# Optimization experiments

Hardware: AMD Instinct MI355X
Metric: run time of the kernel (lower is better)

The kernel has to match this reference:

```python
import jax, jax.numpy as jnp
import numpy as np
import math

N_EMBD = 1024
N_HEAD = 16
B, T = 4, 2048

def setup_inputs() -> dict:
    key = jax.random.key(0)
    k1, k2, k3, k4 = jax.random.split(key, 4)
    x = jax.random.normal(k1, (B, T, N_EMBD), dtype=jnp.float32)
    # torch Linear weights: [out, in]; init scale ~1/sqrt(in)
    s = 1.0 / math.sqrt(N_EMBD)
    W_attn = jax.random.normal(k2, (3 * N_EMBD, N_EMBD), dtype=jnp.float32) * s
    W_proj = jax.random.normal(k3, (N_EMBD, N_EMBD), dtype=jnp.float32) * s
    b_proj = jax.random.normal(k4, (N_EMBD,), dtype=jnp.float32) * s
    return {"x": x, "W_attn": W_attn, "W_proj": W_proj, "b_proj": b_proj}

def reference(x, W_attn, W_proj, b_proj):
    Bx, Tx, C = x.shape
    hd = C // N_HEAD
    qkv = jnp.einsum('btc,oc->bto', x, W_attn)  # [B,T,3C]
    q, k, v = jnp.split(qkv, 3, axis=2)
    # [B, H, T, hd]
    q = q.reshape(Bx, Tx, N_HEAD, hd).transpose(0, 2, 1, 3)
    k = k.reshape(Bx, Tx, N_HEAD, hd).transpose(0, 2, 1, 3)
    v = v.reshape(Bx, Tx, N_HEAD, hd).transpose(0, 2, 1, 3)
    # NOTE: source divides by (1/sqrt(hd)) => MULTIPLIES by sqrt(hd). Faithful.
    att = jnp.einsum('bhqd,bhkd->bhqk', q, k) * jnp.sqrt(jnp.float32(hd))
    causal = jnp.tril(jnp.ones((Tx, Tx), dtype=bool))
    att = jnp.where(causal[None, None, :, :], att, -jnp.inf)
    att = jax.nn.softmax(att, axis=-1)
    y = jnp.einsum('bhqk,bhkd->bhqd', att, v)
    y = y.transpose(0, 2, 1, 3).reshape(Bx, Tx, C)
    y = jnp.einsum('btc,oc->bto', y, W_proj) + b_proj
    return y  # dropout is identity in eval
```

## Files before the change

### kernel.cpp

```cpp
#include <hip/hip_runtime.h>
#include <math.h>

#define BATCH 4
#define TSEQ  2048
#define CEMB  1024
#define NHEAD 16
#define HD    64
#define MROWS (BATCH * TSEQ)
#define QSCALE 11.5415603271f

typedef _Float16 half8 __attribute__((ext_vector_type(8)));
typedef _Float16 half4 __attribute__((ext_vector_type(4)));
typedef _Float16 half2 __attribute__((ext_vector_type(2)));
typedef float    floatx4 __attribute__((ext_vector_type(4)));

#define GLOBAL_AS __attribute__((address_space(1)))
#define LDS_AS    __attribute__((address_space(3)))

__device__ __forceinline__ void lds_dma16(const _Float16* g, _Float16* l) {
    __builtin_amdgcn_global_load_lds((const GLOBAL_AS unsigned int*)g,
                                     (LDS_AS unsigned int*)l, 16, 0, 0);
}

__device__ __forceinline__ float fast_exp2(float x) {
    float r; asm("v_exp_f32 %0, %1" : "=v"(r) : "v"(x)); return r;
}

__device__ __forceinline__ half4 pack4(float a0, float a1, float a2, float a3) {
    half2 lo = __builtin_bit_cast(half2, __builtin_amdgcn_cvt_pkrtz(a0, a1));
    half2 hi = __builtin_bit_cast(half2, __builtin_amdgcn_cvt_pkrtz(a2, a3));
    return (half4){lo[0], lo[1], hi[0], hi[1]};
}

__global__ __launch_bounds__(256)
void cvt_fp16(const float* __restrict__ x, const float* __restrict__ wa,
              const float* __restrict__ wp, _Float16* __restrict__ x16,
              _Float16* __restrict__ wa16, _Float16* __restrict__ wp16)
{
    const int n1 = (BATCH * TSEQ * CEMB) / 4;
    const int n2 = (3 * CEMB * CEMB) / 4;
    int i = blockIdx.x * 256 + threadIdx.x;
    const float* src; _Float16* dst; int j;
    if (i < n1)            { src = x;  dst = x16;  j = i; }
    else if (i < n1 + n2)  { src = wa; dst = wa16; j = i - n1; }
    else                   { src = wp; dst = wp16; j = i - n1 - n2; }
    float4 v = ((const float4*)src)[j];
    half4 h = { (_Float16)v.x, (_Float16)v.y, (_Float16)v.z, (_Float16)v.w };
    ((half4*)dst)[j] = h;
}

__device__ __forceinline__ void stage32(const _Float16* __restrict__ gbase,
                                        _Float16* __restrict__ lds,
                                        int row0, int kk, int tid)
{
#pragma unroll
    for (int p = 0; p < 2; ++p) {
        int ci  = p * 256 + tid;
        int row = ci >> 2, pcc = ci & 3;
        int c   = pcc ^ (row & 3);
        lds_dma16(gbase + (size_t)(row0 + row) * CEMB + kk + c * 8, lds + ci * 8);
    }
}

__global__ __launch_bounds__(256)
void qkv_gemm(const _Float16* __restrict__ A, const _Float16* __restrict__ B,
              _Float16* __restrict__ q16, _Float16* __restrict__ k16,
              _Float16* __restrict__ v16)
{
    __shared__ __align__(16) _Float16 smem[16384];
    const int tid = threadIdx.x, lane = tid & 63, wave = tid >> 6;
    const int wm = wave & 1, wn = wave >> 1;
    const int L  = blockIdx.x + 24 * blockIdx.y;
    const int jj = L >> 3;
    const int m0 = ((L & 7) + 8 * (jj & 7)) * 128;
    const int n0 = (jj >> 3) * 128;
    const int l15 = lane & 15, quad = lane >> 4;

    floatx4 acc[4][4];
#pragma unroll
    for (int i = 0; i < 4; ++i)
#pragma unroll
        for (int j = 0; j < 4; ++j) acc[i][j] = (floatx4){0.f, 0.f, 0.f, 0.f};

    stage32(A, smem, m0, 0, tid);
    stage32(B, smem + 8192, n0, 0, tid);
    for (int kt = 0; kt < 32; ++kt) {
        const int cur = kt & 1;
        _Float16* Asc = smem + cur * 4096;
        _Float16* Bsc = smem + 8192 + cur * 4096;
        __syncthreads();
        if (kt < 31) {
            stage32(A, smem + (cur ^ 1) * 4096, m0, (kt + 1) * 32, tid);
            stage32(B, smem + 8192 + (cur ^ 1) * 4096, n0, (kt + 1) * 32, tid);
        }
        half8 af[4], bf[4];
#pragma unroll
        for (int mt = 0; mt < 4; ++mt) {
            int row = wm * 64 + mt * 16 + l15;
            af[mt] = *(const half8*)(Asc + row * 32 + (quad ^ (row & 3)) * 8);
        }
#pragma unroll
        for (int nt = 0; nt < 4; ++nt) {
            int row = wn * 64 + nt * 16 + l15;
            bf[nt] = *(const half8*)(Bsc + row * 32 + (quad ^ (row & 3)) * 8);
        }
#pragma unroll
        for (int mt = 0; mt < 4; ++mt)
#pragma unroll
            for (int nt = 0; nt < 4; ++nt)
                acc[mt][nt] = __builtin_amdgcn_mfma_f32_16x16x32_f16(af[mt], bf[nt], acc[mt][nt], 0, 0, 0);
    }

    __syncthreads();
    const int rbase = quad << 2;
    if (n0 < 2 * CEMB) {
        const float scale = (n0 < CEMB) ? QSCALE : 1.0f;
#pragma unroll
        for (int mt = 0; mt < 4; ++mt)
#pragma unroll
            for (int nt = 0; nt < 4; ++nt)
#pragma unroll
                for (int r = 0; r < 4; ++r) {
                    int t = wm * 64 + mt * 16 + rbase + r;
                    int n = wn * 64 + nt * 16 + l15;
                    int pc = (n >> 3) ^ (t & 15);
                    smem[t * 128 + pc * 8 + (n & 7)] = (_Float16)(acc[mt][nt][r] * scale);
                }
        __syncthreads();
        const int chunk = tid & 7;
#pragma unroll
        for (int i = 0; i < 8; ++i) {
            int gr = (tid >> 3) + i * 32;
            int seg = gr >> 7, t = gr & 127;
            int pc = (seg * 8 + chunk) ^ (t & 15);
            half8 v = *(const half8*)(smem + t * 128 + pc * 8);
            int gm = m0 + t, b = gm >> 11, tt = gm & (TSEQ - 1);
            int gnb = n0 + seg * 64;
            _Float16* dst;
            if (n0 < CEMB) {
                int h = gnb >> 6;
                dst = q16 + (((size_t)(b * NHEAD + h)) * TSEQ + tt) * HD;
            } else {
                int h = (gnb - CEMB) >> 6;
                dst = k16 + (((size_t)(b * NHEAD + h)) * TSEQ + tt) * HD;
            }
            *(half8*)(dst + chunk * 8) = v;
        }
    } else {
#pragma unroll
        for (int mt = 0; mt < 4; ++mt)
#pragma unroll
            for (int nt = 0; nt < 4; ++nt)
#pragma unroll
                for (int r = 0; r < 4; ++r) {
                    int t = wm * 64 + mt * 16 + rbase + r;
                    int n = wn * 64 + nt * 16 + l15;
                    int pc = (t >> 3) ^ (n & 15);
                    smem[n * 128 + pc * 8 + (t & 7)] = (_Float16)acc[mt][nt][r];
                }
        __syncthreads();
        const int chunk = tid & 15;
        const int b = m0 >> 11, tblk = m0 & (TSEQ - 1);
#pragma unroll
        for (int i = 0; i < 8; ++i) {
            int row = (tid >> 4) + i * 16;
            int pc = chunk ^ (row & 15);
            half8 v = *(const half8*)(smem + row * 128 + pc * 8);
            int c2 = n0 - 2 * CEMB + row;
            int h = c2 >> 6, d = c2 & 63;
            *(half8*)(v16 + (((size_t)(b * NHEAD + h)) * HD + d) * TSEQ + tblk + chunk * 8) = v;
        }
    }
}

__device__ __forceinline__ void attn_tile(
    const half8& qf0, const half8& qf1,
    float& m_i, float& l_i, floatx4 (&o)[4],
    const _Float16* __restrict__ Ks, const _Float16* __restrict__ Vs,
    bool domask, int l15, int quad, int relq)
{
    floatx4 s[4];
#pragma unroll
    for (int nt = 0; nt < 4; ++nt) {
        int row = nt * 16 + l15;
        int pc0 = quad ^ (row & 7);
        half8 kf0 = *(const half8*)(Ks + row * 64 + pc0 * 8);
        half8 kf1 = *(const half8*)(Ks + row * 64 + (pc0 ^ 4) * 8);
        floatx4 z = (floatx4){0.f, 0.f, 0.f, 0.f};
        z = __builtin_amdgcn_mfma_f32_16x16x32_f16(kf0, qf0, z, 0, 0, 0);
        z = __builtin_amdgcn_mfma_f32_16x16x32_f16(kf1, qf1, z, 0, 0, 0);
        s[nt] = z;
    }
    if (domask) {
#pragma unroll
        for (int nt = 0; nt < 4; ++nt)
#pragma unroll
            for (int r = 0; r < 4; ++r)
                if (nt * 16 + quad * 4 + r > relq) s[nt][r] = -INFINITY;
    }
    float pmax = -INFINITY;
#pragma unroll
    for (int nt = 0; nt < 4; ++nt)
        pmax = fmaxf(pmax, fmaxf(fmaxf(s[nt][0], s[nt][1]), fmaxf(s[nt][2], s[nt][3])));
    if (!__all(pmax <= m_i)) {
        float mx = fmaxf(m_i, pmax);
        mx = fmaxf(mx, __shfl_xor(mx, 16, 64));
        mx = fmaxf(mx, __shfl_xor(mx, 32, 64));
        float alpha = fast_exp2(m_i - mx);
        m_i = mx;
        l_i *= alpha;
#pragma unroll
        for (int mt = 0; mt < 4; ++mt)
#pragma unroll
            for (int r = 0; r < 4; ++r) o[mt][r] *= alpha;
    }
    float rs = 0.f;
    half4 p[4];
#pragma unroll
    for (int nt = 0; nt < 4; ++nt) {
        float p0 = fast_exp2(s[nt][0] - m_i), p1 = fast_exp2(s[nt][1] - m_i);
        float p2 = fast_exp2(s[nt][2] - m_i), p3 = fast_exp2(s[nt][3] - m_i);
        rs += (p0 + p1) + (p2 + p3);
        p[nt] = pack4(p0, p1, p2, p3);
    }
    l_i += rs;
#pragma unroll
    for (int mt = 0; mt < 4; ++mt) {
        int d = mt * 16 + l15;
#pragma unroll
        for (int nt = 0; nt < 4; ++nt) {
            int pc = (2 * nt + (quad >> 1)) ^ (d & 7);
            half4 vf = *(const half4*)(Vs + d * 64 + pc * 8 + (quad & 1) * 4);
            o[mt] = __builtin_amdgcn_mfma_f32_16x16x16f16(vf, p[nt], o[mt], 0, 0, 0);
        }
    }
}

__device__ __forceinline__ void attn_tile2(
    const half8& qA0, const half8& qA1, const half8& qB0, const half8& qB1,
    float& mAi, float& lAi, floatx4 (&oA)[4],
    float& mBi, float& lBi, floatx4 (&oB)[4],
    const _Float16* __restrict__ Ks, const _Float16* __restrict__ Vs,
    bool maskA, int l15, int quad, int relq)
{
    floatx4 sA[4], sB[4];
#pragma unroll
    for (int nt = 0; nt < 4; ++nt) {
        int row = nt * 16 + l15;
        int pc0 = quad ^ (row & 7);
        half8 kf0 = *(const half8*)(Ks + row * 64 + pc0 * 8);
        half8 kf1 = *(const half8*)(Ks + row * 64 + (pc0 ^ 4) * 8);
        floatx4 zA = (floatx4){0.f, 0.f, 0.f, 0.f};
        floatx4 zB = (floatx4){0.f, 0.f, 0.f, 0.f};
        zA = __builtin_amdgcn_mfma_f32_16x16x32_f16(kf0, qA0, zA, 0, 0, 0);
        zB = __builtin_amdgcn_mfma_f32_16x16x32_f16(kf0, qB0, zB, 0, 0, 0);
        zA = __builtin_amdgcn_mfma_f32_16x16x32_f16(kf1, qA1, zA, 0, 0, 0);
        zB = __builtin_amdgcn_mfma_f32_16x16x32_f16(kf1, qB1, zB, 0, 0, 0);
        sA[nt] = zA; sB[nt] = zB;
    }
    if (maskA) {
#pragma unroll
        for (int nt = 0; nt < 4; ++nt)
#pragma unroll
            for (int r = 0; r < 4; ++r)
                if (nt * 16 + quad * 4 + r > relq) sA[nt][r] = -INFINITY;
    }
    float pA = -INFINITY, pB = -INFINITY;
#pragma unroll
    for (int nt = 0; nt < 4; ++nt) {
        pA = fmaxf(pA, fmaxf(fmaxf(sA[nt][0], sA[nt][1]), fmaxf(sA[nt][2], sA[nt][3])));
        pB = fmaxf(pB, fmaxf(fmaxf(sB[nt][0], sB[nt][1]), fmaxf(sB[nt][2], sB[nt][3])));
    }
    if (!__all((pA <= mAi) && (pB <= mBi))) {
        float mxA = fmaxf(mAi, pA), mxB = fmaxf(mBi, pB);
        mxA = fmaxf(mxA, __shfl_xor(mxA, 16, 64));
        mxB = fmaxf(mxB, __shfl_xor(mxB, 16, 64));
        mxA = fmaxf(mxA, __shfl_xor(mxA, 32, 64));
        mxB = fmaxf(mxB, __shfl_xor(mxB, 32, 64));
        float alA = fast_exp2(mAi - mxA);
        float alB = fast_exp2(mBi - mxB);
        mAi = mxA; mBi = mxB;
        lAi *= alA; lBi *= alB;
#pragma unroll
        for (int mt = 0; mt < 4; ++mt)
#pragma unroll
            for (int r = 0; r < 4; ++r) { oA[mt][r] *= alA; oB[mt][r] *= alB; }
    }
    float rsA = 0.f, rsB = 0.f;
    half4 pAh[4], pBh[4];
#pragma unroll
    for (int nt = 0; nt < 4; ++nt) {
        float a0 = fast_exp2(sA[nt][0] - mAi), b0 = fast_exp2(sB[nt][0] - mBi);
        float a1 = fast_exp2(sA[nt][1] - mAi), b1 = fast_exp2(sB[nt][1] - mBi);
        float a2 = fast_exp2(sA[nt][2] - mAi), b2 = fast_exp2(sB[nt][2] - mBi);
        float a3 = fast_exp2(sA[nt][3] - mAi), b3 = fast_exp2(sB[nt][3] - mBi);
        rsA += (a0 + a1) + (a2 + a3);
        rsB += (b0 + b1) + (b2 + b3);
        pAh[nt] = pack4(a0, a1, a2, a3);
        pBh[nt] = pack4(b0, b1, b2, b3);
    }
    lAi += rsA; lBi += rsB;
#pragma unroll
    for (int mt = 0; mt < 4; ++mt) {
        int d = mt * 16 + l15;
#pragma unroll
        for (int nt = 0; nt < 4; ++nt) {
            int pc = (2 * nt + (quad >> 1)) ^ (d & 7);
            half4 vf = *(const half4*)(Vs + d * 64 + pc * 8 + (quad & 1) * 4);
            oA[mt] = __builtin_amdgcn_mfma_f32_16x16x16f16(vf, pAh[nt], oA[mt], 0, 0, 0);
            oB[mt] = __builtin_amdgcn_mfma_f32_16x16x16f16(vf, pBh[nt], oB[mt], 0, 0, 0);
        }
    }
}

__global__ __launch_bounds__(256)
void attn_fwd(const _Float16* __restrict__ q16, const _Float16* __restrict__ k16,
              const _Float16* __restrict__ v16, _Float16* __restrict__ o16)
{
    __shared__ __align__(16) _Float16 Ks[2][64 * 64];
    __shared__ __align__(16) _Float16 Vs[2][64 * 64];
    const int tid = threadIdx.x, lane = tid & 63, wave = tid >> 6;
    const int l15 = lane & 15, quad = lane >> 4;

    const int L   = blockIdx.x + 16 * blockIdx.y;
    const int qtA = (L >> 3) & 15;
    const int bh  = (L & 7) + ((L >> 7) << 3);
    const int qtB = 31 - qtA;
    const int b = bh >> 4, h = bh & 15;
    const int q0A = qtA * 64, q0B = qtB * 64;
    const _Float16* qp = q16 + (size_t)bh * TSEQ * HD;
    const _Float16* kp = k16 + (size_t)bh * TSEQ * HD;
    const _Float16* vp = v16 + (size_t)bh * HD * TSEQ;

    const int relq = wave * 16 + l15;
    half8 qA0 = *(const half8*)(qp + (size_t)(q0A + relq) * HD + quad * 8);
    half8 qA1 = *(const half8*)(qp + (size_t)(q0A + relq) * HD + 32 + quad * 8);
    half8 qB0 = *(const half8*)(qp + (size_t)(q0B + relq) * HD + quad * 8);
    half8 qB1 = *(const half8*)(qp + (size_t)(q0B + relq) * HD + 32 + quad * 8);

    float mA = -INFINITY, lA = 0.f, mB = -INFINITY, lB = 0.f;
    floatx4 oA[4], oB[4];
#pragma unroll
    for (int mt = 0; mt < 4; ++mt) { oA[mt] = (floatx4){0.f,0.f,0.f,0.f}; oB[mt] = (floatx4){0.f,0.f,0.f,0.f}; }

#define STAGE_KV(kt0, buf)                                                     \
    {                                                                          \
        _Float16* kd = Ks[buf];                                                \
        _Float16* vd = Vs[buf];                                                \
        _Pragma("unroll")                                                      \
        for (int p = 0; p < 2; ++p) {                                          \
            int ci = p * 256 + tid;                                            \
            int row = ci >> 3;                                                 \
            int c2 = (ci & 7) ^ (row & 7);                                     \
            lds_dma16(kp + (size_t)((kt0) + row) * HD + c2 * 8, kd + ci * 8);  \
            lds_dma16(vp + (size_t)row * TSEQ + (kt0) + c2 * 8, vd + ci * 8);  \
        }                                                                      \
    }

    STAGE_KV(0, 0);
    for (int kt = 0; kt <= qtA; ++kt) {
        const int cur = kt & 1;
        __syncthreads();
        STAGE_KV((kt + 1) * 64, cur ^ 1);
        attn_tile2(qA0, qA1, qB0, qB1, mA, lA, oA, mB, lB, oB,
                   Ks[cur], Vs[cur], (kt == qtA), l15, quad, relq);
    }
    for (int kt = qtA + 1; kt <= qtB; ++kt) {
        const int cur = kt & 1;
        __syncthreads();
        if (kt < qtB) STAGE_KV((kt + 1) * 64, cur ^ 1);
        attn_tile(qB0, qB1, mB, lB, oB, Ks[cur], Vs[cur], (kt == qtB), l15, quad, relq);
    }
#undef STAGE_KV

    lA += __shfl_xor(lA, 16, 64); lA += __shfl_xor(lA, 32, 64);
    lB += __shfl_xor(lB, 16, 64); lB += __shfl_xor(lB, 32, 64);
    const float invA = 1.f / lA, invB = 1.f / lB;
    const size_t baseA = ((size_t)(b * TSEQ + q0A + relq)) * CEMB + h * HD + quad * 4;
    const size_t baseB = ((size_t)(b * TSEQ + q0B + relq)) * CEMB + h * HD + quad * 4;
#pragma unroll
    for (int mt = 0; mt < 4; ++mt) {
        half4 ha = { (_Float16)(oA[mt][0] * invA), (_Float16)(oA[mt][1] * invA),
                     (_Float16)(oA[mt][2] * invA), (_Float16)(oA[mt][3] * invA) };
        half4 hb = { (_Float16)(oB[mt][0] * invB), (_Float16)(oB[mt][1] * invB),
                     (_Float16)(oB[mt][2] * invB), (_Float16)(oB[mt][3] * invB) };
        *(half4*)(o16 + baseA + mt * 16) = ha;
        *(half4*)(o16 + baseB + mt * 16) = hb;
    }
}

__global__ __launch_bounds__(256)
void proj_gemm(const _Float16* __restrict__ A, const _Float16* __restrict__ B,
               const float* __restrict__ bias, float* __restrict__ out)
{
    __shared__ __align__(16) _Float16 smem[16384];
    const int tid = threadIdx.x, lane = tid & 63, wave = tid >> 6;
    const int wm = wave & 1, wn = wave >> 1;
    const int L  = blockIdx.x + 8 * blockIdx.y;
    const int jj = L >> 3;
    const int m0 = ((L & 7) + 8 * (jj & 7)) * 128;
    const int n0 = (jj >> 3) * 128;
    const int l15 = lane & 15, quad = lane >> 4;

    floatx4 acc[4][4];
#pragma unroll
    for (int i = 0; i < 4; ++i)
#pragma unroll
        for (int j = 0; j < 4; ++j) acc[i][j] = (floatx4){0.f, 0.f, 0.f, 0.f};

    stage32(A, smem, m0, 0, tid);
    stage32(B, smem + 8192, n0, 0, tid);
    for (int kt = 0; kt < 32; ++kt) {
        const int cur = kt & 1;
        _Float16* Asc = smem + cur * 4096;
        _Float16* Bsc = smem + 8192 + cur * 4096;
        __syncthreads();
        if (kt < 31) {
            stage32(A, smem + (cur ^ 1) * 4096, m0, (kt + 1) * 32, tid);
            stage32(B, smem + 8192 + (cur ^ 1) * 4096, n0, (kt + 1) * 32, tid);
        }
        half8 af[4], bf[4];
#pragma unroll
        for (int mt = 0; mt < 4; ++mt) {
            int row = wm * 64 + mt * 16 + l15;
            af[mt] = *(const half8*)(Asc + row * 32 + (quad ^ (row & 3)) * 8);
        }
#pragma unroll
        for (int nt = 0; nt < 4; ++nt) {
            int row = wn * 64 + nt * 16 + l15;
            bf[nt] = *(const half8*)(Bsc + row * 32 + (quad ^ (row & 3)) * 8);
        }
#pragma unroll
        for (int mt = 0; mt < 4; ++mt)
#pragma unroll
            for (int nt = 0; nt < 4; ++nt)
                acc[mt][nt] = __builtin_amdgcn_mfma_f32_16x16x32_f16(af[mt], bf[nt], acc[mt][nt], 0, 0, 0);
    }

    const int rbase = quad << 2;
#pragma unroll
    for (int mt = 0; mt < 4; ++mt)
#pragma unroll
        for (int nt = 0; nt < 4; ++nt) {
            int gn = n0 + wn * 64 + nt * 16 + l15;
            float bb = bias[gn];
#pragma unroll
            for (int r = 0; r < 4; ++r) {
                int gm = m0 + wm * 64 + mt * 16 + rbase + r;
                out[(size_t)gm * CEMB + gn] = acc[mt][nt][r] + bb;
            }
        }
}

extern "C" void kernel_launch(void* const* d_in, const int* in_sizes, int n_in,
                              void* d_out, int out_size, void* d_ws, size_t ws_size,
                              hipStream_t stream) {
    const float* x     = (const float*)d_in[0];
    const float* Wattn = (const float*)d_in[1];
    const float* Wproj = (const float*)d_in[2];
    const float* bproj = (const float*)d_in[3];
    float* out = (float*)d_out;

    const size_t nx  = (size_t)BATCH * TSEQ * CEMB;
    const size_t nwa = (size_t)3 * CEMB * CEMB;
    const size_t nwp = (size_t)CEMB * CEMB;
    const size_t per = (size_t)BATCH * NHEAD * TSEQ * HD;

    _Float16* x16    = (_Float16*)d_ws;
    _Float16* wa16   = x16 + nx;
    _Float16* wp16   = wa16 + nwa;
    _Float16* q16    = wp16 + nwp;
    _Float16* k16    = q16 + per;
    _Float16* v16    = k16 + per;
    _Float16* attn16 = x16;

    const int nconv = (int)((nx + nwa + nwp) / 4);
    cvt_fp16<<<nconv / 256, 256, 0, stream>>>(x, Wattn, Wproj, x16, wa16, wp16);
    qkv_gemm<<<dim3(3 * CEMB / 128, MROWS / 128), 256, 0, stream>>>(x16, wa16, q16, k16, v16);
    attn_fwd<<<dim3(16, BATCH * NHEAD), 256, 0, stream>>>(q16, k16, v16, attn16);
    proj_gemm<<<dim3(CEMB / 128, MROWS / 128), 256, 0, stream>>>(attn16, wp16, bproj, out);
}
```

Measured before the change: 276.0 us.

## Split QKV projection into large-tile pipelined Q/K GEMM and separate V GEMM

Replaces the single 128x128-tile QKV GEMM with two kernels. The Q/K part becomes a 512-thread, 256x256-tile GEMM. It uses a 64-wide K step, double-buffered LDS DMA staging interleaved across four phases per K tile, explicit vmcnt waits, and s_setprio around the MFMA bursts. V keeps the old 128-tile kernel with its transposed store. The goal is more data reuse per tile and better overlap of global loads with MFMA work. The cost is 128KB of LDS per block, which limits occupancy, and a much more complex hand-scheduled pipeline.

```diff
diff --git a/kernel.cpp b/kernel.cpp
--- a/kernel.cpp
+++ b/kernel.cpp
@@ -62,18 +62,155 @@
     }
 }
 
+__device__ __forceinline__ void stage_half(const _Float16* __restrict__ g,
+                                           _Float16* __restrict__ lds,
+                                           int row0, int kk, int tid)
+{
+#pragma unroll
+    for (int p = 0; p < 2; ++p) {
+        int ci  = p * 512 + tid;
+        int row = ci >> 3;
+        int c   = (ci & 7) ^ (row & 7);
+        lds_dma16(g + (size_t)(row0 + row) * CEMB + kk + c * 8, lds + ci * 8);
+    }
+}
+
+__global__ __launch_bounds__(512, 2)
+void qk_gemm(const _Float16* __restrict__ A, const _Float16* __restrict__ B,
+             _Float16* __restrict__ q16, _Float16* __restrict__ k16)
+{
+    __shared__ __align__(16) _Float16 smem[65536];
+    const int tid = threadIdx.x, lane = tid & 63, wv = tid >> 6;
+    const int wm = wv & 1, wn = wv >> 1;
+    const int l15 = lane & 15, quad = lane >> 4;
+
+    const int L  = blockIdx.x + 8 * blockIdx.y;
+    const int m0 = ((L & 7) * 4 + ((L >> 3) & 3)) * 256;
+    const int n0 = (L >> 5) * 256;
+
+    floatx4 acc[8][4];
+#pragma unroll
+    for (int i = 0; i < 8; ++i)
+#pragma unroll
+        for (int j = 0; j < 4; ++j) acc[i][j] = (floatx4){0.f, 0.f, 0.f, 0.f};
+
+#define STG_A(t, hf) stage_half(A, smem + (((t)&1)*2 + (hf))*8192, m0 + (hf)*128, (t)*64, tid)
+#define STG_B(t, hf) stage_half(B, smem + 32768 + (((t)&1)*2 + (hf))*8192, n0 + (hf)*128, (t)*64, tid)
+#define NOSTG ((void)0)
+#define WAIT4 asm volatile("s_waitcnt vmcnt(4)" ::: "memory")
+#define WAIT0 asm volatile("s_waitcnt vmcnt(0)" ::: "memory")
+#define NOWAIT ((void)0)
+
+    STG_B(0, 0); STG_B(0, 1); STG_A(0, 0); STG_A(0, 1);
+    STG_B(1, 0); STG_B(1, 1);
+    WAIT4;
+    __builtin_amdgcn_s_barrier();
+
+#define PHASE(t, qd, STAGE_STMT, WAIT_STMT)                                   \
+    {                                                                         \
+        const _Float16* Ab = smem + (((t)&1)*2 + wm) * 8192;                  \
+        const _Float16* Bb = smem + 32768 + (((t)&1)*2 + (wn >> 1)) * 8192;   \
+        half8 af[2][2];                                                       \
+        _Pragma("unroll")                                                     \
+        for (int i = 0; i < 2; ++i) {                                         \
+            int row = ((qd)*2 + i)*16 + l15;                                  \
+            _Pragma("unroll")                                                 \
+            for (int ks = 0; ks < 2; ++ks)                                    \
+                af[i][ks] = *(const half8*)(Ab + row*64 + (((ks*4 + quad) ^ (row & 7)) << 3)); \
+        }                                                                     \
+        if ((qd) == 0) {                                                      \
+            _Pragma("unroll")                                                 \
+            for (int ni = 0; ni < 4; ++ni) {                                  \
+                int row = (wn & 1)*64 + ni*16 + l15;                          \
+                _Pragma("unroll")                                             \
+                for (int ks = 0; ks < 2; ++ks)                                \
+                    bfr[ni][ks] = *(const half8*)(Bb + row*64 + (((ks*4 + quad) ^ (row & 7)) << 3)); \
+            }                                                                 \
+        }                                                                     \
+        STAGE_STMT;                                                           \
+        __builtin_amdgcn_s_barrier();                                         \
+        __builtin_amdgcn_s_setprio(1);                                        \
+        _Pragma("unroll")                                                     \
+        for (int i = 0; i < 2; ++i)                                           \
+            _Pragma("unroll")                                                 \
+            for (int ni = 0; ni < 4; ++ni) {                                  \
+                acc[(qd)*2+i][ni] = __builtin_amdgcn_mfma_f32_16x16x32_f16(af[i][0], bfr[ni][0], acc[(qd)*2+i][ni], 0, 0, 0); \
+                acc[(qd)*2+i][ni] = __builtin_amdgcn_mfma_f32_16x16x32_f16(af[i][1], bfr[ni][1], acc[(qd)*2+i][ni], 0, 0, 0); \
+            }                                                                 \
+        __builtin_amdgcn_s_setprio(0);                                        \
+        WAIT_STMT;                                                            \
+        __builtin_amdgcn_s_barrier();                                         \
+    }
+
+    for (int j = 0; j < 7; ++j) {
+        const int t0 = 2*j, t1 = 2*j + 1;
+        half8 bfr[4][2];
+        PHASE(t0, 0, STG_A(t1, 0),     NOWAIT);
+        PHASE(t0, 1, STG_A(t1, 1),     NOWAIT);
+        PHASE(t0, 2, STG_B(t0 + 2, 0), NOWAIT);
+        PHASE(t0, 3, STG_B(t0 + 2, 1), WAIT4);
+        PHASE(t1, 0, STG_A(t0 + 2, 0), NOWAIT);
+        PHASE(t1, 1, STG_A(t0 + 2, 1), NOWAIT);
+        PHASE(t1, 2, STG_B(t1 + 2, 0), NOWAIT);
+        PHASE(t1, 3, STG_B(t1 + 2, 1), WAIT4);
+    }
+    {
+        half8 bfr[4][2];
+        PHASE(14, 0, STG_A(15, 0), NOWAIT);
+        PHASE(14, 1, STG_A(15, 1), NOWAIT);
+        PHASE(14, 2, NOSTG,        NOWAIT);
+        PHASE(14, 3, NOSTG,        WAIT0);
+        PHASE(15, 0, NOSTG,        NOWAIT);
+        PHASE(15, 1, NOSTG,        NOWAIT);
+        PHASE(15, 2, NOSTG,        NOWAIT);
+        PHASE(15, 3, NOSTG,        NOWAIT);
+    }
+#undef PHASE
+#undef STG_A
+#undef STG_B
+
+    __builtin_amdgcn_s_barrier();
+    const float scale = (n0 < CEMB) ? QSCALE : 1.0f;
+    const int rbase = quad << 2;
+#pragma unroll
+    for (int mi = 0; mi < 8; ++mi)
+#pragma unroll
+        for (int ni = 0; ni < 4; ++ni)
+#pragma unroll
+            for (int r = 0; r < 4; ++r) {
+                int t = wm*128 + mi*16 + rbase + r;
+                int n = wn*64 + ni*16 + l15;
+                int pc = (n >> 3) ^ (t & 31);
+                smem[t*256 + pc*8 + (n & 7)] = (_Float16)(acc[mi][ni][r] * scale);
+            }
+    asm volatile("s_waitcnt lgkmcnt(0)" ::: "memory");
+    __builtin_amdgcn_s_barrier();
+    const int chunk = tid & 31;
+    _Float16* dstb = (n0 < CEMB) ? q16 : k16;
+    const int nbase = n0 - ((n0 < CEMB) ? 0 : CEMB);
+#pragma unroll
+    for (int i = 0; i < 16; ++i) {
+        int t = (tid >> 5) + i*16;
+        int pc = chunk ^ (t & 31);
+        half8 v = *(const half8*)(smem + t*256 + pc*8);
+        int gm = m0 + t, b = gm >> 11, tt = gm & (TSEQ - 1);
+        int gn = nbase + chunk*8;
+        int h = gn >> 6, d = gn & 63;
+        *(half8*)(dstb + (((size_t)(b * NHEAD + h)) * TSEQ + tt) * HD + d) = v;
+    }
+}
+
 __global__ __launch_bounds__(256)
-void qkv_gemm(const _Float16* __restrict__ A, const _Float16* __restrict__ B,
-              _Float16* __restrict__ q16, _Float16* __restrict__ k16,
-              _Float16* __restrict__ v16)
+void v_gemm(const _Float16* __restrict__ A, const _Float16* __restrict__ B,
+            _Float16* __restrict__ v16)
 {
     __shared__ __align__(16) _Float16 smem[16384];
     const int tid = threadIdx.x, lane = tid & 63, wave = tid >> 6;
     const int wm = wave & 1, wn = wave >> 1;
-    const int L  = blockIdx.x + 24 * blockIdx.y;
+    const int L  = blockIdx.x + 8 * blockIdx.y;
     const int jj = L >> 3;
     const int m0 = ((L & 7) + 8 * (jj & 7)) * 128;
-    const int n0 = (jj >> 3) * 128;
+    const int n0 = 2 * CEMB + (jj >> 3) * 128;
     const int l15 = lane & 15, quad = lane >> 4;
 
     floatx4 acc[4][4];
@@ -113,63 +250,28 @@
 
     __syncthreads();
     const int rbase = quad << 2;
-    if (n0 < 2 * CEMB) {
-        const float scale = (n0 < CEMB) ? QSCALE : 1.0f;
-#pragma unroll
-        for (int mt = 0; mt < 4; ++mt)
-#pragma unroll
-            for (int nt = 0; nt < 4; ++nt)
-#pragma unroll
-                for (int r = 0; r < 4; ++r) {
-                    int t = wm * 64 + mt * 16 + rbase + r;
-                    int n = wn * 64 + nt * 16 + l15;
-                    int pc = (n >> 3) ^ (t & 15);
-                    smem[t * 128 + pc * 8 + (n & 7)] = (_Float16)(acc[mt][nt][r] * scale);
-                }
-        __syncthreads();
-        const int chunk = tid & 7;
-#pragma unroll
-        for (int i = 0; i < 8; ++i) {
-            int gr = (tid >> 3) + i * 32;
-            int seg = gr >> 7, t = gr & 127;
-            int pc = (seg * 8 + chunk) ^ (t & 15);
-            half8 v = *(const half8*)(smem + t * 128 + pc * 8);
-            int gm = m0 + t, b = gm >> 11, tt = gm & (TSEQ - 1);
-            int gnb = n0 + seg * 64;
-            _Float16* dst;
-            if (n0 < CEMB) {
-                int h = gnb >> 6;
-                dst = q16 + (((size_t)(b * NHEAD + h)) * TSEQ + tt) * HD;
-            } else {
-                int h = (gnb - CEMB) >> 6;
-                dst = k16 + (((size_t)(b * NHEAD + h)) * TSEQ + tt) * HD;
+#pragma unroll
+    for (int mt = 0; mt < 4; ++mt)
+#pragma unroll
+        for (int nt = 0; nt < 4; ++nt)
+#pragma unroll
+            for (int r = 0; r < 4; ++r) {
+                int t = wm * 64 + mt * 16 + rbase + r;
+                int n = wn * 64 + nt * 16 + l15;
+                int pc = (t >> 3) ^ (n & 15);
+                smem[n * 128 + pc * 8 + (t & 7)] = (_Float16)acc[mt][nt][r];
             }
-            *(half8*)(dst + chunk * 8) = v;
-        }
-    } else {
-#pragma unroll
-        for (int mt = 0; mt < 4; ++mt)
-#pragma unroll
-            for (int nt = 0; nt < 4; ++nt)
-#pragma unroll
-                for (int r = 0; r < 4; ++r) {
-                    int t = wm * 64 + mt * 16 + rbase + r;
-                    int n = wn * 64 + nt * 16 + l15;
-                    int pc = (t >> 3) ^ (n & 15);
-                    smem[n * 128 + pc * 8 + (t & 7)] = (_Float16)acc[mt][nt][r];
-                }
-        __syncthreads();
-        const int chunk = tid & 15;
-        const int b = m0 >> 11, tblk = m0 & (TSEQ - 1);
-#pragma unroll
-        for (int i = 0; i < 8; ++i) {
-            int row = (tid >> 4) + i * 16;
-            int pc = chunk ^ (row & 15);
-            half8 v = *(const half8*)(smem + row * 128 + pc * 8);
-            int c2 = n0 - 2 * CEMB + row;
-            int h = c2 >> 6, d = c2 & 63;
-            *(half8*)(v16 + (((size_t)(b * NHEAD + h)) * HD + d) * TSEQ + tblk + chunk * 8) = v;
-        }
+    __syncthreads();
+    const int chunk = tid & 15;
+    const int b = m0 >> 11, tblk = m0 & (TSEQ - 1);
+#pragma unroll
+    for (int i = 0; i < 8; ++i) {
+        int row = (tid >> 4) + i * 16;
+        int pc = chunk ^ (row & 15);
+        half8 v = *(const half8*)(smem + row * 128 + pc * 8);
+        int c2 = n0 - 2 * CEMB + row;
+        int h = c2 >> 6, d = c2 & 63;
+        *(half8*)(v16 + (((size_t)(b * NHEAD + h)) * HD + d) * TSEQ + tblk + chunk * 8) = v;
     }
 }
 
@@ -476,7 +578,8 @@
 
     const int nconv = (int)((nx + nwa + nwp) / 4);
     cvt_fp16<<<nconv / 256, 256, 0, stream>>>(x, Wattn, Wproj, x16, wa16, wp16);
-    qkv_gemm<<<dim3(3 * CEMB / 128, MROWS / 128), 256, 0, stream>>>(x16, wa16, q16, k16, v16);
+    qk_gemm<<<dim3(8, 32), 512, 0, stream>>>(x16, wa16, q16, k16);
+    v_gemm<<<dim3(8, 64), 256, 0, stream>>>(x16, wa16, v16);
     attn_fwd<<<dim3(16, BATCH * NHEAD), 256, 0, stream>>>(q16, k16, v16, attn16);
     proj_gemm<<<dim3(CEMB / 128, MROWS / 128), 256, 0, stream>>>(attn16, wp16, bproj, out);
 }
```

After: 270.0 us. -2.2%, faster.
